# Performance work log

Measured on AMD Instinct MI355X. Metric: run time of the kernel, lower is better.

Reference implementation:

```python
import jax, jax.numpy as jnp
import numpy as np

EMBED = 100
BATCH = 4096
NUM_NEG = 256
U, P, W, RP, B, C = 30000, 50000, 100000, 50000, 5000, 1000


def _tab(k, v, e=EMBED):
    r = 0.5 / e
    w = jax.random.uniform(k, (v + 1, e), minval=-r, maxval=r, dtype=jnp.float32)
    return w.at[-1].set(0.0)  # padding row is zeros, as in torch code


def setup_inputs() -> dict:
    key = jax.random.key(0)
    ks = jax.random.split(key, 10)
    inp = {
        'user_emb': _tab(ks[0], U),
        'product_emb': _tab(ks[1], P),
        'word_emb': _tab(ks[2], W),
        'brand_emb': _tab(ks[3], B),
        'category_emb': _tab(ks[4], C),
        'rproduct_emb': _tab(ks[5], RP),
        'rel_vecs': jax.random.uniform(ks[6], (8, EMBED), minval=-0.5 / EMBED, maxval=0.5 / EMBED, dtype=jnp.float32),
        'purchase_bias': jnp.zeros((P + 1,), jnp.float32),
        'mentions_bias': jnp.zeros((W + 1,), jnp.float32),
        'describe_bias': jnp.zeros((W + 1,), jnp.float32),
        'produced_bias': jnp.zeros((B + 1,), jnp.float32),
        'belongs_bias': jnp.zeros((C + 1,), jnp.float32),
        'also_bought_bias': jnp.zeros((RP + 1,), jnp.float32),
        'also_viewed_bias': jnp.zeros((RP + 1,), jnp.float32),
        'together_bias': jnp.zeros((RP + 1,), jnp.float32),
    }
    # batch_idxs columns: (u, p, w, b, c, rp1, rp2, rp3), each in its own vocab range
    col_max = [U, P, W, B, C, RP, RP, RP]
    cols = [jax.random.randint(jax.random.fold_in(ks[7], i), (BATCH,), 0, m) for i, m in enumerate(col_max)]
    inp['batch_idxs'] = jnp.stack(cols, axis=1)
    # deterministic stand-in for torch.multinomial negative sampling, one row per relation
    neg_max = [P, W, W, B, C, RP, RP, RP]
    negs = [jax.random.randint(jax.random.fold_in(ks[8], i), (NUM_NEG,), 0, m) for i, m in enumerate(neg_max)]
    inp['neg_idxs'] = jnp.stack(negs, axis=0)
    return inp


def _neg_loss(head_tab, tail_tab, rvec, bias_tab, h, t, n):
    hv = head_tab[h]                      # [B,E] gather
    ex = hv + rvec                        # [B,E]
    tv = tail_tab[t]                      # [B,E]
    bias = bias_tab[t]                    # [B]
    pos = jnp.sum(ex * tv, axis=-1) + bias  # bmm([B,1,E],[B,E,1]) == rowwise dot
    nv = tail_tab[n]                      # [N,E]
    neg = jnp.einsum('be,ne->bn', ex, nv) + bias[:, None]  # [B,N]
    pos_loss = -jax.nn.log_sigmoid(pos)   # == -log(sigmoid(pos)), stable
    neg_loss = -jax.nn.log_sigmoid(-neg).sum(axis=1)
    return (pos_loss + neg_loss).mean()


def reference(batch_idxs, neg_idxs, user_emb, product_emb, word_emb, brand_emb,
              category_emb, rproduct_emb, rel_vecs, purchase_bias, mentions_bias,
              describe_bias, produced_bias, belongs_bias, also_bought_bias,
              also_viewed_bias, together_bias):
    # (head_tab, tail_tab, bias_tab, head_col, tail_col) per relation, in original order
    rels = [
        (user_emb, product_emb, purchase_bias, 0, 1),
        (user_emb, word_emb, mentions_bias, 0, 2),
        (product_emb, word_emb, describe_bias, 1, 2),
        (product_emb, brand_emb, produced_bias, 1, 3),
        (product_emb, category_emb, belongs_bias, 1, 4),
        (product_emb, rproduct_emb, also_bought_bias, 1, 5),
        (product_emb, rproduct_emb, also_viewed_bias, 1, 6),
        (product_emb, rproduct_emb, together_bias, 1, 7),
    ]
    loss = jnp.float32(0.0)
    for r, (ht, tt, bt, hc, tc) in enumerate(rels):
        loss = loss + _neg_loss(ht, tt, rel_vecs[r], bt,
                                batch_idxs[:, hc], batch_idxs[:, tc], neg_idxs[r])
    return loss
```

## Files before the change

### kernel.cpp

```cpp
#include <hip/hip_runtime.h>


#define EMBED   100
#define BATCH   4096
#define NUM_NEG 256
#define BM      64
#define BN      256
#define PITCH   104

typedef __attribute__((ext_vector_type(8))) short s8;
typedef __attribute__((ext_vector_type(4))) short s4;
typedef __attribute__((ext_vector_type(4))) float f4;

struct RelP {
    const float* head;
    const float* tail;
    const float* bias;
    int hc, tc;
};

struct Params {
    RelP rel[8];
    const float* rel_vecs;
    const int*   batch_idxs;
    const int*   neg_idxs;
    float*       out;
};

__device__ __forceinline__ float softplus_f(float x) {
    float e = __expf(-fabsf(x));
    return fmaxf(x, 0.0f) + __logf(1.0f + e);
}

__device__ __forceinline__ unsigned short bf16_rne(float f) {
    unsigned u = __float_as_uint(f);
    u += 0x7FFFu + ((u >> 16) & 1u);
    return (unsigned short)(u >> 16);
}

__device__ __forceinline__ float bf16_to_f(short s) {
    return __uint_as_float(((unsigned)(unsigned short)s) << 16);
}

__device__ __forceinline__ s4 pack4(float4 f) {
    s4 v = { (short)bf16_rne(f.x), (short)bf16_rne(f.y),
             (short)bf16_rne(f.z), (short)bf16_rne(f.w) };
    return v;
}

__launch_bounds__(256, 2)
__global__ void ke_kernel(Params p) {
    const int bid = blockIdx.x;
    const int r   = bid & 7;
    const int rb  = bid >> 3;
    const int tid = threadIdx.x;

    __shared__ __align__(16) short As[BM * PITCH];
    __shared__ __align__(16) short Bs[BN * PITCH];

    const RelP rp = p.rel[r];

    const int g    = tid & 7;
    const int rloc = tid >> 3;

    const float4* rv4 = (const float4*)(p.rel_vecs + r * EMBED);
#pragma unroll
    for (int pass = 0; pass < 2; ++pass) {
        const int row  = pass * 32 + rloc;
        const int grow = rb * BM + row;
        const int h = p.batch_idxs[grow * 8 + rp.hc];
        const float4* s4p = (const float4*)(rp.head + (size_t)h * EMBED);
        short* dst = As + row * PITCH;
#pragma unroll
        for (int t = 0; t < 3; ++t) {
            const int j = g + 8 * t;
            float4 f = s4p[j];
            const float4 a = rv4[j];
            f.x += a.x; f.y += a.y; f.z += a.z; f.w += a.w;
            *(s4*)(dst + 4 * j) = pack4(f);
        }
        if (g == 0) {
            const int ti = p.batch_idxs[grow * 8 + rp.tc];
            const unsigned short extra = bf16_rne(rp.bias[ti]);
            float4 f = s4p[24];
            const float4 a = rv4[24];
            f.x += a.x; f.y += a.y; f.z += a.z; f.w += a.w;
            s8 v = { (short)bf16_rne(f.x), (short)bf16_rne(f.y),
                     (short)bf16_rne(f.z), (short)bf16_rne(f.w),
                     (short)extra, 0, 0, 0 };
            *(s8*)(dst + 96) = v;
        }
    }

#pragma unroll
    for (int pass = 0; pass < 8; ++pass) {
        const int row = pass * 32 + rloc;
        const int n = p.neg_idxs[r * NUM_NEG + row];
        const float4* s4p = (const float4*)(rp.tail + (size_t)n * EMBED);
        short* dst = Bs + row * PITCH;
#pragma unroll
        for (int t = 0; t < 3; ++t) {
            const int j = g + 8 * t;
            *(s4*)(dst + 4 * j) = pack4(s4p[j]);
        }
        if (g == 0) {
            float4 f = s4p[24];
            s8 v = { (short)bf16_rne(f.x), (short)bf16_rne(f.y),
                     (short)bf16_rne(f.z), (short)bf16_rne(f.w),
                     (short)0x3F80, 0, 0, 0 };
            *(s8*)(dst + 96) = v;
        }
    }

    const int prow_l = tid >> 2;
    const int pp     = tid & 3;
    const int pgrow  = rb * BM + prow_l;
    const int pt     = p.batch_idxs[pgrow * 8 + rp.tc];
    const float* ptail = rp.tail + (size_t)pt * EMBED;
    const float  pbias = rp.bias[pt];

    __syncthreads();

    const int wave = tid >> 6;
    const int lane = tid & 63;
    const int li   = lane & 15;
    const int q    = lane >> 4;
    const int wm   = wave >> 1;
    const int wn   = wave & 1;

    f4 acc[2][8];
#pragma unroll
    for (int i = 0; i < 2; ++i)
#pragma unroll
        for (int j = 0; j < 8; ++j)
            acc[i][j] = (f4){0.f, 0.f, 0.f, 0.f};

    const short* Ab = As + (wm * 32 + li) * PITCH;
    const short* Bb = Bs + (wn * 128 + li) * PITCH;

#pragma unroll
    for (int s = 0; s < 3; ++s) {
        const int co = 8 * (q + 4 * s);
        s8 a[2], b[8];
        a[0] = *(const s8*)(Ab + co);
        a[1] = *(const s8*)(Ab + 16 * PITCH + co);
#pragma unroll
        for (int j = 0; j < 8; ++j)
            b[j] = *(const s8*)(Bb + j * 16 * PITCH + co);
#pragma unroll
        for (int i = 0; i < 2; ++i)
#pragma unroll
            for (int j = 0; j < 8; ++j)
                acc[i][j] = __builtin_amdgcn_mfma_f32_16x16x32_bf16(a[i], b[j], acc[i][j], 0, 0, 0);
    }
    {
        const s8 z = {0, 0, 0, 0, 0, 0, 0, 0};
        s8 a[2], b[8];
        a[0] = *(const s8*)(Ab + 96);
        a[1] = *(const s8*)(Ab + 16 * PITCH + 96);
#pragma unroll
        for (int j = 0; j < 8; ++j) {
            b[j] = *(const s8*)(Bb + j * 16 * PITCH + 96);
            b[j] = q ? z : b[j];
        }
#pragma unroll
        for (int i = 0; i < 2; ++i)
#pragma unroll
            for (int j = 0; j < 8; ++j)
                acc[i][j] = __builtin_amdgcn_mfma_f32_16x16x32_bf16(a[i], b[j], acc[i][j], 0, 0, 0);
    }

    float local = 0.0f;
#pragma unroll
    for (int i = 0; i < 2; ++i)
#pragma unroll
        for (int j = 0; j < 8; ++j) {
            local += softplus_f(acc[i][j].x);
            local += softplus_f(acc[i][j].y);
            local += softplus_f(acc[i][j].z);
            local += softplus_f(acc[i][j].w);
        }

    {
        const short* exr = As + prow_l * PITCH;
        const float4* tv = (const float4*)ptail;
        float d0 = 0.f, d1 = 0.f, d2 = 0.f, d3 = 0.f;
#pragma unroll
        for (int t = 0; t < 6; ++t) {
            const int j = pp + 4 * t;
            const s4 e = *(const s4*)(exr + 4 * j);
            const float4 t0 = tv[j];
            d0 = fmaf(bf16_to_f(e.x), t0.x, d0);
            d1 = fmaf(bf16_to_f(e.y), t0.y, d1);
            d2 = fmaf(bf16_to_f(e.z), t0.z, d2);
            d3 = fmaf(bf16_to_f(e.w), t0.w, d3);
        }
        if (pp == 0) {
            const s4 e = *(const s4*)(exr + 96);
            const float4 t0 = tv[24];
            d0 = fmaf(bf16_to_f(e.x), t0.x, d0);
            d1 = fmaf(bf16_to_f(e.y), t0.y, d1);
            d2 = fmaf(bf16_to_f(e.z), t0.z, d2);
            d3 = fmaf(bf16_to_f(e.w), t0.w, d3);
        }
        float d = (d0 + d1) + (d2 + d3);
        d += __shfl_xor(d, 1, 64);
        d += __shfl_xor(d, 2, 64);
        if (pp == 0) local += softplus_f(-(d + pbias));
    }

#pragma unroll
    for (int off = 32; off > 0; off >>= 1)
        local += __shfl_down(local, off, 64);

    __syncthreads();
    float* wsum = (float*)Bs;
    if ((tid & 63) == 0) wsum[tid >> 6] = local;
    __syncthreads();
    if (tid == 0) {
        const float s = (wsum[0] + wsum[1]) + (wsum[2] + wsum[3]);
        atomicAdd(p.out, s * (1.0f / BATCH));
    }
}

extern "C" void kernel_launch(void* const* d_in, const int* in_sizes, int n_in,
                              void* d_out, int out_size, void* d_ws, size_t ws_size,
                              hipStream_t stream) {
    const float* user  = (const float*)d_in[0];
    const float* prod  = (const float*)d_in[1];
    const float* word  = (const float*)d_in[2];
    const float* brand = (const float*)d_in[3];
    const float* cat   = (const float*)d_in[4];
    const float* rprod = (const float*)d_in[5];

    Params p;
    p.rel_vecs   = (const float*)d_in[6];
    p.batch_idxs = (const int*)d_in[15];
    p.neg_idxs   = (const int*)d_in[16];
    p.out        = (float*)d_out;

    p.rel[0] = {user, prod,  (const float*)d_in[7],  0, 1};
    p.rel[1] = {user, word,  (const float*)d_in[8],  0, 2};
    p.rel[2] = {prod, word,  (const float*)d_in[9],  1, 2};
    p.rel[3] = {prod, brand, (const float*)d_in[10], 1, 3};
    p.rel[4] = {prod, cat,   (const float*)d_in[11], 1, 4};
    p.rel[5] = {prod, rprod, (const float*)d_in[12], 1, 5};
    p.rel[6] = {prod, rprod, (const float*)d_in[13], 1, 6};
    p.rel[7] = {prod, rprod, (const float*)d_in[14], 1, 7};

    hipMemsetAsync(d_out, 0, sizeof(float), stream);
    ke_kernel<<<512, 256, 0, stream>>>(p);
}
```

Baseline: 152.2 us.

## Process all eight relations per block with shared staged head embeddings

Each block now covers 16 batch rows and loops over all eight relations, instead of one relation per 64-row tile. The user, product and word rows for those 16 batch rows are staged once in shared memory and reused as heads and as positive tails. The aim is to cut repeated head gathers across relations. In exchange, the 256 negative rows are re-gathered and converted for every relation in every block, which is about four times more negative-table traffic overall. The MFMA tiles shrink to 16 rows, the grid halves, and each relation iteration adds block barriers.

```diff
diff --git a/kernel.cpp b/kernel.cpp
--- a/kernel.cpp
+++ b/kernel.cpp
@@ -4,23 +4,23 @@
 #define EMBED   100
 #define BATCH   4096
 #define NUM_NEG 256
-#define BM      64
-#define BN      256
+#define PF      100
 #define PITCH   104
 
 typedef __attribute__((ext_vector_type(8))) short s8;
-typedef __attribute__((ext_vector_type(4))) short s4;
+typedef __attribute__((ext_vector_type(4))) short s4v;
 typedef __attribute__((ext_vector_type(4))) float f4;
 
 struct RelP {
-    const float* head;
     const float* tail;
     const float* bias;
-    int hc, tc;
+    int tc;
 };
 
 struct Params {
     RelP rel[8];
+    const float* user;
+    const float* prod;
     const float* rel_vecs;
     const int*   batch_idxs;
     const int*   neg_idxs;
@@ -42,180 +42,188 @@
     return __uint_as_float(((unsigned)(unsigned short)s) << 16);
 }
 
-__device__ __forceinline__ s4 pack4(float4 f) {
-    s4 v = { (short)bf16_rne(f.x), (short)bf16_rne(f.y),
-             (short)bf16_rne(f.z), (short)bf16_rne(f.w) };
+__device__ __forceinline__ s4v pack4(float4 f) {
+    s4v v = { (short)bf16_rne(f.x), (short)bf16_rne(f.y),
+              (short)bf16_rne(f.z), (short)bf16_rne(f.w) };
     return v;
 }
 
-__launch_bounds__(256, 2)
+__launch_bounds__(256, 1)
 __global__ void ke_kernel(Params p) {
     const int bid = blockIdx.x;
-    const int r   = bid & 7;
-    const int rb  = bid >> 3;
+    const int R0  = bid * 16;
     const int tid = threadIdx.x;
 
-    __shared__ __align__(16) short As[BM * PITCH];
-    __shared__ __align__(16) short Bs[BN * PITCH];
-
-    const RelP rp = p.rel[r];
+    __shared__ __align__(16) float U[16 * PF];
+    __shared__ __align__(16) float P[16 * PF];
+    __shared__ __align__(16) float W[16 * PF];
+    __shared__ __align__(16) short Ac[16 * PITCH];
+    __shared__ __align__(16) short Bs[NUM_NEG * PITCH];
+    __shared__ float wsum[4];
+
+    const int row  = tid >> 4;
+    const int j    = tid & 15;
+    const int grow = R0 + row;
+
+    {
+        const int c0 = p.batch_idxs[grow * 8 + 0];
+        const float4* s = (const float4*)(p.user + (size_t)c0 * EMBED);
+        float4* d = (float4*)(U + row * PF);
+        d[j] = s[j];
+        if (j < 9) d[j + 16] = s[j + 16];
+    }
+    {
+        const int c1 = p.batch_idxs[grow * 8 + 1];
+        const float4* s = (const float4*)(p.prod + (size_t)c1 * EMBED);
+        float4* d = (float4*)(P + row * PF);
+        d[j] = s[j];
+        if (j < 9) d[j + 16] = s[j + 16];
+    }
+    {
+        const int c2 = p.batch_idxs[grow * 8 + 2];
+        const float4* s = (const float4*)(p.rel[1].tail + (size_t)c2 * EMBED);
+        float4* d = (float4*)(W + row * PF);
+        d[j] = s[j];
+        if (j < 9) d[j + 16] = s[j + 16];
+    }
+
+    __syncthreads();
 
     const int g    = tid & 7;
     const int rloc = tid >> 3;
-
-    const float4* rv4 = (const float4*)(p.rel_vecs + r * EMBED);
-#pragma unroll
-    for (int pass = 0; pass < 2; ++pass) {
-        const int row  = pass * 32 + rloc;
-        const int grow = rb * BM + row;
-        const int h = p.batch_idxs[grow * 8 + rp.hc];
-        const float4* s4p = (const float4*)(rp.head + (size_t)h * EMBED);
-        short* dst = As + row * PITCH;
-#pragma unroll
-        for (int t = 0; t < 3; ++t) {
-            const int j = g + 8 * t;
-            float4 f = s4p[j];
-            const float4 a = rv4[j];
-            f.x += a.x; f.y += a.y; f.z += a.z; f.w += a.w;
-            *(s4*)(dst + 4 * j) = pack4(f);
-        }
-        if (g == 0) {
-            const int ti = p.batch_idxs[grow * 8 + rp.tc];
-            const unsigned short extra = bf16_rne(rp.bias[ti]);
-            float4 f = s4p[24];
-            const float4 a = rv4[24];
-            f.x += a.x; f.y += a.y; f.z += a.z; f.w += a.w;
-            s8 v = { (short)bf16_rne(f.x), (short)bf16_rne(f.y),
-                     (short)bf16_rne(f.z), (short)bf16_rne(f.w),
-                     (short)extra, 0, 0, 0 };
-            *(s8*)(dst + 96) = v;
-        }
-    }
-
-#pragma unroll
-    for (int pass = 0; pass < 8; ++pass) {
-        const int row = pass * 32 + rloc;
-        const int n = p.neg_idxs[r * NUM_NEG + row];
-        const float4* s4p = (const float4*)(rp.tail + (size_t)n * EMBED);
-        short* dst = Bs + row * PITCH;
-#pragma unroll
-        for (int t = 0; t < 3; ++t) {
-            const int j = g + 8 * t;
-            *(s4*)(dst + 4 * j) = pack4(s4p[j]);
-        }
-        if (g == 0) {
-            float4 f = s4p[24];
-            s8 v = { (short)bf16_rne(f.x), (short)bf16_rne(f.y),
-                     (short)bf16_rne(f.z), (short)bf16_rne(f.w),
-                     (short)0x3F80, 0, 0, 0 };
-            *(s8*)(dst + 96) = v;
-        }
-    }
-
-    const int prow_l = tid >> 2;
-    const int pp     = tid & 3;
-    const int pgrow  = rb * BM + prow_l;
-    const int pt     = p.batch_idxs[pgrow * 8 + rp.tc];
-    const float* ptail = rp.tail + (size_t)pt * EMBED;
-    const float  pbias = rp.bias[pt];
-
-    __syncthreads();
-
     const int wave = tid >> 6;
     const int lane = tid & 63;
     const int li   = lane & 15;
     const int q    = lane >> 4;
-    const int wm   = wave >> 1;
-    const int wn   = wave & 1;
-
-    f4 acc[2][8];
-#pragma unroll
-    for (int i = 0; i < 2; ++i)
-#pragma unroll
-        for (int j = 0; j < 8; ++j)
-            acc[i][j] = (f4){0.f, 0.f, 0.f, 0.f};
-
-    const short* Ab = As + (wm * 32 + li) * PITCH;
-    const short* Bb = Bs + (wn * 128 + li) * PITCH;
-
-#pragma unroll
-    for (int s = 0; s < 3; ++s) {
-        const int co = 8 * (q + 4 * s);
-        s8 a[2], b[8];
-        a[0] = *(const s8*)(Ab + co);
-        a[1] = *(const s8*)(Ab + 16 * PITCH + co);
-#pragma unroll
-        for (int j = 0; j < 8; ++j)
-            b[j] = *(const s8*)(Bb + j * 16 * PITCH + co);
-#pragma unroll
-        for (int i = 0; i < 2; ++i)
-#pragma unroll
-            for (int j = 0; j < 8; ++j)
-                acc[i][j] = __builtin_amdgcn_mfma_f32_16x16x32_bf16(a[i], b[j], acc[i][j], 0, 0, 0);
-    }
-    {
-        const s8 z = {0, 0, 0, 0, 0, 0, 0, 0};
-        s8 a[2], b[8];
-        a[0] = *(const s8*)(Ab + 96);
-        a[1] = *(const s8*)(Ab + 16 * PITCH + 96);
-#pragma unroll
-        for (int j = 0; j < 8; ++j) {
-            b[j] = *(const s8*)(Bb + j * 16 * PITCH + 96);
-            b[j] = q ? z : b[j];
-        }
-#pragma unroll
-        for (int i = 0; i < 2; ++i)
-#pragma unroll
-            for (int j = 0; j < 8; ++j)
-                acc[i][j] = __builtin_amdgcn_mfma_f32_16x16x32_bf16(a[i], b[j], acc[i][j], 0, 0, 0);
-    }
 
     float local = 0.0f;
-#pragma unroll
-    for (int i = 0; i < 2; ++i)
-#pragma unroll
-        for (int j = 0; j < 8; ++j) {
-            local += softplus_f(acc[i][j].x);
-            local += softplus_f(acc[i][j].y);
-            local += softplus_f(acc[i][j].z);
-            local += softplus_f(acc[i][j].w);
-        }
-
-    {
-        const short* exr = As + prow_l * PITCH;
-        const float4* tv = (const float4*)ptail;
-        float d0 = 0.f, d1 = 0.f, d2 = 0.f, d3 = 0.f;
-#pragma unroll
-        for (int t = 0; t < 6; ++t) {
-            const int j = pp + 4 * t;
-            const s4 e = *(const s4*)(exr + 4 * j);
-            const float4 t0 = tv[j];
-            d0 = fmaf(bf16_to_f(e.x), t0.x, d0);
-            d1 = fmaf(bf16_to_f(e.y), t0.y, d1);
-            d2 = fmaf(bf16_to_f(e.z), t0.z, d2);
-            d3 = fmaf(bf16_to_f(e.w), t0.w, d3);
-        }
-        if (pp == 0) {
-            const s4 e = *(const s4*)(exr + 96);
-            const float4 t0 = tv[24];
-            d0 = fmaf(bf16_to_f(e.x), t0.x, d0);
-            d1 = fmaf(bf16_to_f(e.y), t0.y, d1);
-            d2 = fmaf(bf16_to_f(e.z), t0.z, d2);
-            d3 = fmaf(bf16_to_f(e.w), t0.w, d3);
-        }
-        float d = (d0 + d1) + (d2 + d3);
-        d += __shfl_xor(d, 1, 64);
-        d += __shfl_xor(d, 2, 64);
-        if (pp == 0) local += softplus_f(-(d + pbias));
+
+#pragma unroll
+    for (int r = 0; r < 8; ++r) {
+        const RelP rp = p.rel[r];
+        const float* hrow = (r < 2 ? U : P) + row * PF;
+        const float* rv   = p.rel_vecs + r * EMBED;
+
+        {
+            short* dst = Ac + row * PITCH;
+            {
+                float4 f = *(const float4*)(hrow + 4 * j);
+                const float4 a = *(const float4*)(rv + 4 * j);
+                f.x += a.x; f.y += a.y; f.z += a.z; f.w += a.w;
+                *(s4v*)(dst + 4 * j) = pack4(f);
+            }
+            if (j < 9) {
+                const int c = j + 16;
+                float4 f = *(const float4*)(hrow + 4 * c);
+                const float4 a = *(const float4*)(rv + 4 * c);
+                f.x += a.x; f.y += a.y; f.z += a.z; f.w += a.w;
+                *(s4v*)(dst + 4 * c) = pack4(f);
+            }
+            if (j == 15) {
+                const int ti = p.batch_idxs[grow * 8 + rp.tc];
+                s4v v = { (short)bf16_rne(rp.bias[ti]), 0, 0, 0 };
+                *(s4v*)(dst + 100) = v;
+            }
+        }
+
+#pragma unroll
+        for (int pass = 0; pass < 8; ++pass) {
+            const int brow = pass * 32 + rloc;
+            const int n = p.neg_idxs[r * NUM_NEG + brow];
+            const float* s = rp.tail + (size_t)n * EMBED;
+            short* dst = Bs + brow * PITCH;
+#pragma unroll
+            for (int t = 0; t < 3; ++t) {
+                const int c = g + 8 * t;
+                *(s4v*)(dst + 4 * c) = pack4(*(const float4*)(s + 4 * c));
+            }
+            if (g == 0) {
+                float4 f = *(const float4*)(s + 96);
+                s8 v = { (short)bf16_rne(f.x), (short)bf16_rne(f.y),
+                         (short)bf16_rne(f.z), (short)bf16_rne(f.w),
+                         (short)0x3F80, 0, 0, 0 };
+                *(s8*)(dst + 96) = v;
+            }
+        }
+
+        __syncthreads();
+
+        f4 acc[4];
+#pragma unroll
+        for (int jj = 0; jj < 4; ++jj) acc[jj] = (f4){0.f, 0.f, 0.f, 0.f};
+
+        const short* Ab = Ac + li * PITCH;
+        const short* Bb = Bs + (wave * 64 + li) * PITCH;
+
+#pragma unroll
+        for (int s2 = 0; s2 < 3; ++s2) {
+            const int co = 8 * (q + 4 * s2);
+            const s8 a = *(const s8*)(Ab + co);
+#pragma unroll
+            for (int jj = 0; jj < 4; ++jj) {
+                const s8 b = *(const s8*)(Bb + jj * 16 * PITCH + co);
+                acc[jj] = __builtin_amdgcn_mfma_f32_16x16x32_bf16(a, b, acc[jj], 0, 0, 0);
+            }
+        }
+        {
+            const s8 z = {0, 0, 0, 0, 0, 0, 0, 0};
+            const s8 a = *(const s8*)(Ab + 96);
+#pragma unroll
+            for (int jj = 0; jj < 4; ++jj) {
+                s8 b = *(const s8*)(Bb + jj * 16 * PITCH + 96);
+                b = q ? z : b;
+                acc[jj] = __builtin_amdgcn_mfma_f32_16x16x32_bf16(a, b, acc[jj], 0, 0, 0);
+            }
+        }
+
+#pragma unroll
+        for (int jj = 0; jj < 4; ++jj) {
+            local += softplus_f(acc[jj].x);
+            local += softplus_f(acc[jj].y);
+            local += softplus_f(acc[jj].z);
+            local += softplus_f(acc[jj].w);
+        }
+
+        {
+            const int ti = p.batch_idxs[grow * 8 + rp.tc];
+            const short* exr = Ac + row * PITCH;
+            const float* tsrc = (r == 0) ? (P + row * PF)
+                              : (r <= 2) ? (W + row * PF)
+                              : (rp.tail + (size_t)ti * EMBED);
+            float d0 = 0.f, d1 = 0.f, d2 = 0.f, d3 = 0.f;
+            {
+                const s4v e = *(const s4v*)(exr + 4 * j);
+                const float4 t0 = *(const float4*)(tsrc + 4 * j);
+                d0 = fmaf(bf16_to_f(e.x), t0.x, d0);
+                d1 = fmaf(bf16_to_f(e.y), t0.y, d1);
+                d2 = fmaf(bf16_to_f(e.z), t0.z, d2);
+                d3 = fmaf(bf16_to_f(e.w), t0.w, d3);
+            }
+            if (j < 9) {
+                const int c = j + 16;
+                const s4v e = *(const s4v*)(exr + 4 * c);
+                const float4 t0 = *(const float4*)(tsrc + 4 * c);
+                d0 = fmaf(bf16_to_f(e.x), t0.x, d0);
+                d1 = fmaf(bf16_to_f(e.y), t0.y, d1);
+                d2 = fmaf(bf16_to_f(e.z), t0.z, d2);
+                d3 = fmaf(bf16_to_f(e.w), t0.w, d3);
+            }
+            float d = (d0 + d1) + (d2 + d3);
+            d += __shfl_xor(d, 1, 64);
+            d += __shfl_xor(d, 2, 64);
+            d += __shfl_xor(d, 4, 64);
+            d += __shfl_xor(d, 8, 64);
+            if (j == 0) local += softplus_f(-(d + rp.bias[ti]));
+        }
+
+        __syncthreads();
     }
 
 #pragma unroll
     for (int off = 32; off > 0; off >>= 1)
         local += __shfl_down(local, off, 64);
 
-    __syncthreads();
-    float* wsum = (float*)Bs;
-    if ((tid & 63) == 0) wsum[tid >> 6] = local;
+    if (lane == 0) wsum[wave] = local;
     __syncthreads();
     if (tid == 0) {
         const float s = (wsum[0] + wsum[1]) + (wsum[2] + wsum[3]);
@@ -234,20 +242,22 @@
     const float* rprod = (const float*)d_in[5];
 
     Params p;
+    p.user       = user;
+    p.prod       = prod;
     p.rel_vecs   = (const float*)d_in[6];
     p.batch_idxs = (const int*)d_in[15];
     p.neg_idxs   = (const int*)d_in[16];
     p.out        = (float*)d_out;
 
-    p.rel[0] = {user, prod,  (const float*)d_in[7],  0, 1};
-    p.rel[1] = {user, word,  (const float*)d_in[8],  0, 2};
-    p.rel[2] = {prod, word,  (const float*)d_in[9],  1, 2};
-    p.rel[3] = {prod, brand, (const float*)d_in[10], 1, 3};
-    p.rel[4] = {prod, cat,   (const float*)d_in[11], 1, 4};
-    p.rel[5] = {prod, rprod, (const float*)d_in[12], 1, 5};
-    p.rel[6] = {prod, rprod, (const float*)d_in[13], 1, 6};
-    p.rel[7] = {prod, rprod, (const float*)d_in[14], 1, 7};
+    p.rel[0] = {prod,  (const float*)d_in[7],  1};
+    p.rel[1] = {word,  (const float*)d_in[8],  2};
+    p.rel[2] = {word,  (const float*)d_in[9],  2};
+    p.rel[3] = {brand, (const float*)d_in[10], 3};
+    p.rel[4] = {cat,   (const float*)d_in[11], 4};
+    p.rel[5] = {rprod, (const float*)d_in[12], 5};
+    p.rel[6] = {rprod, (const float*)d_in[13], 6};
+    p.rel[7] = {rprod, (const float*)d_in[14], 7};
 
     hipMemsetAsync(d_out, 0, sizeof(float), stream);
-    ke_kernel<<<512, 256, 0, stream>>>(p);
-}
+    ke_kernel<<<256, 256, 0, stream>>>(p);
+}
```

Result: slower. 210.7 us (+38.4%).
